# Performance work log

Measured on AMD Instinct MI355X. Metric: run time of the kernel, lower is better.

The kernel has to match this reference:

```python
import jax, jax.numpy as jnp
import numpy as np
from jax import lax

B, T, H, F, K, NB, MAXLEN = 32, 1024, 384, 384, 3, 256, 2048


def _ln(x, g, b, eps=1e-5):
    m = jnp.mean(x, axis=-1, keepdims=True)
    v = jnp.var(x, axis=-1, keepdims=True)
    return (x - m) * lax.rsqrt(v + eps) * g + b


def _conv(x, w, b):
    # x: (B, T, Cin), w: (K, Cin, Cout); SAME padding == torch padding=(K-1)//2 for K=3, stride 1
    y = lax.conv_general_dilated(x, w, (1,), 'SAME', dimension_numbers=('NWC', 'WIO', 'NWC'))
    return y + b


def _predictor(x, mask, w1, b1, g1, be1, w2, b2, g2, be2, wo, bo):
    h = _ln(jax.nn.relu(_conv(x, w1, b1)), g1, be1)
    h = _ln(jax.nn.relu(_conv(h, w2, b2)), g2, be2)
    out = jnp.einsum('btf,f->bt', h, wo) + bo  # Linear(F -> 1).squeeze(-1)
    return jnp.where(mask, 0.0, out)


def _length_regulate(x, dur, max_len):
    # vectorized equivalent of torch per-sample expand+cat+pad
    csum = jnp.cumsum(dur, axis=1)                      # (B, T)
    total = csum[:, -1]                                 # (B,) = mel_len
    frames = jnp.arange(max_len)                        # (M,)
    # frame f belongs to phoneme i with csum[i-1] <= f < csum[i]
    idx = jax.vmap(lambda c: jnp.searchsorted(c, frames, side='right'))(csum)  # (B, M)
    idx = jnp.clip(idx, 0, x.shape[1] - 1)
    out = jnp.take_along_axis(x, idx[:, :, None], axis=1)                      # (B, M, H)
    valid = (frames[None, :] < total[:, None]).astype(x.dtype)                 # zero-pad tail
    return out * valid[:, :, None], total


def setup_inputs() -> dict:
    key = jax.random.key(0)
    ks = iter(jax.random.split(key, 64))
    nk = lambda: next(ks)
    d = {}
    d['x'] = jax.random.normal(nk(), (B, T, H), jnp.float32)
    d['src_mask'] = jnp.zeros((B, T), jnp.bool_)
    d['duration'] = jax.random.randint(nk(), (B, T), 0, 4)
    d['max_len'] = MAXLEN
    for p in ('dp', 'pp', 'ep'):
        d[p + '_w1'] = jax.random.normal(nk(), (K, H, F), jnp.float32) * 0.02
        d[p + '_b1'] = jnp.zeros((F,), jnp.float32)
        d[p + '_g1'] = jnp.ones((F,), jnp.float32)
        d[p + '_be1'] = jnp.zeros((F,), jnp.float32)
        d[p + '_w2'] = jax.random.normal(nk(), (K, F, F), jnp.float32) * 0.02
        d[p + '_b2'] = jnp.zeros((F,), jnp.float32)
        d[p + '_g2'] = jnp.ones((F,), jnp.float32)
        d[p + '_be2'] = jnp.zeros((F,), jnp.float32)
        d[p + '_wo'] = jax.random.normal(nk(), (F,), jnp.float32) * 0.02
        d[p + '_bo'] = jnp.zeros((1,), jnp.float32)
    d['pitch_bins'] = jnp.linspace(0.0, 1.0, NB - 1, dtype=jnp.float32)
    d['energy_bins'] = jnp.linspace(0.0, 1.0, NB - 1, dtype=jnp.float32)
    d['pitch_emb'] = jax.random.normal(nk(), (NB, H), jnp.float32) * 0.02
    d['energy_emb'] = jax.random.normal(nk(), (NB, H), jnp.float32) * 0.02
    d['pitch_target'] = jax.random.uniform(nk(), (B, T), jnp.float32)
    d['energy_target'] = jax.random.uniform(nk(), (B, T), jnp.float32)
    return d


def reference(x, src_mask, duration, max_len,
              dp_w1, dp_b1, dp_g1, dp_be1, dp_w2, dp_b2, dp_g2, dp_be2, dp_wo, dp_bo,
              pp_w1, pp_b1, pp_g1, pp_be1, pp_w2, pp_b2, pp_g2, pp_be2, pp_wo, pp_bo,
              ep_w1, ep_b1, ep_g1, ep_be1, ep_w2, ep_b2, ep_g2, ep_be2, ep_wo, ep_bo,
              pitch_bins, energy_bins, pitch_emb, energy_emb, pitch_target, energy_target):
    log_dur = _predictor(x, src_mask, dp_w1, dp_b1, dp_g1, dp_be1, dp_w2, dp_b2, dp_g2, dp_be2, dp_wo, dp_bo)
    # phoneme-level pitch (target path: bucketize target, torch.bucketize right=False == searchsorted left)
    pitch_pred = _predictor(x, src_mask, pp_w1, pp_b1, pp_g1, pp_be1, pp_w2, pp_b2, pp_g2, pp_be2, pp_wo, pp_bo)
    x = x + pitch_emb[jnp.searchsorted(pitch_bins, pitch_target, side='left')]
    # phoneme-level energy (predictor sees x AFTER pitch embedding add, as in torch)
    energy_pred = _predictor(x, src_mask, ep_w1, ep_b1, ep_g1, ep_be1, ep_w2, ep_b2, ep_g2, ep_be2, ep_wo, ep_bo)
    x = x + energy_emb[jnp.searchsorted(energy_bins, energy_target, side='left')]
    x_out, mel_len = _length_regulate(x, duration, max_len)
    return (x_out, pitch_pred, energy_pred, log_dur, mel_len)
```

## Files before the change

kernel.cpp:

```cpp
#include <hip/hip_runtime.h>

#define B_ 32
#define T_ 1024
#define C_ 384
#define MAXLEN_ 2048
#define NBINS_ 255
#define WPK1 442368
#define BTC  (32 * 1024 * 384)
#define ARS 392

typedef __attribute__((ext_vector_type(8))) short short8v;
typedef __attribute__((ext_vector_type(4))) float floatx4;

__device__ __forceinline__ unsigned short f2bf(float f) {
    unsigned u = __float_as_uint(f);
    u += 0x7fffu + ((u >> 16) & 1u);
    return (unsigned short)(u >> 16);
}

struct CvP {
    const float* xf;
    const unsigned short* xb;
    const unsigned short* wpk;
    const float* bias[3];
    const float* gamma[3];
    const float* beta[3];
    const float* wo[3];
    const float* bo[3];
    unsigned short* hout;
    float* pred[3];
    const float* pbins;
    const float* pemb;
    const float* ptgt;
    int final_flag;
};

__global__ __launch_bounds__(512, 3) void conv_mfma3(CvP P)
{
    __shared__ unsigned short As[66 * ARS];
    __shared__ int embi[66];
    float* rsum = (float*)As;
    float* rsq  = rsum + 512;
    float* prbuf = rsum + 1024;

    const int tid  = threadIdx.x;
    const int wave = tid >> 6;
    const int lane = tid & 63;
    const int lq   = lane >> 4;
    const int ln   = lane & 15;
    const int p    = blockIdx.x >> 9;
    const int bi   = blockIdx.x & 511;
    const int b    = bi >> 4;
    const int t0   = (bi & 15) << 6;
    const int nb   = wave * 48;

    const unsigned short* bbase =
        P.wpk + (size_t)p * WPK1 + (size_t)(wave * 1536) + (size_t)lane * 8;
    short8v bA[3], bB[3];
#pragma unroll
    for (int nt = 0; nt < 3; ++nt) {
        bA[nt] = *(const short8v*)(bbase + (nt << 9));
        bB[nt] = *(const short8v*)(bbase + 12288 + (nt << 9));
    }

    if (!P.final_flag) {
        const bool fuse_emb = (p == 2);
        if (fuse_emb) {
            if (tid < 66) {
                const int t = t0 - 1 + tid;
                int lo = 0;
                if ((unsigned)t < (unsigned)T_) {
                    const float tg = P.ptgt[(b << 10) + t];
                    int hi = NBINS_;
                    while (lo < hi) {
                        const int mid = (lo + hi) >> 1;
                        if (P.pbins[mid] < tg) lo = mid + 1; else hi = mid;
                    }
                }
                embi[tid] = lo;
            }
            __syncthreads();
        }
        for (int i = tid; i < 66 * 96; i += 512) {
            const int row = i / 96;
            const int c4  = i - row * 96;
            const int t   = t0 - 1 + row;
            uint2 pv = make_uint2(0u, 0u);
            if ((unsigned)t < (unsigned)T_) {
                float4 f = *(const float4*)(P.xf + ((size_t)(b << 10) + t) * C_ + c4 * 4);
                if (fuse_emb) {
                    const float* er = P.pemb + (size_t)embi[row] * C_ + c4 * 4;
                    f.x += er[0]; f.y += er[1]; f.z += er[2]; f.w += er[3];
                }
                asm("v_cvt_pk_bf16_f32 %0, %1, %2" : "=v"(pv.x) : "v"(f.x), "v"(f.y));
                asm("v_cvt_pk_bf16_f32 %0, %1, %2" : "=v"(pv.y) : "v"(f.z), "v"(f.w));
            }
            *(uint2*)&As[row * ARS + c4 * 4] = pv;
        }
    } else {
        const unsigned short* xb = P.xb + (size_t)p * BTC;
        for (int i = tid; i < 66 * 48; i += 512) {
            const int row = i / 48;
            const int c   = i - row * 48;
            const int t   = t0 - 1 + row;
            short8v v = (short8v){0,0,0,0,0,0,0,0};
            if ((unsigned)t < (unsigned)T_)
                v = *(const short8v*)(xb + ((size_t)(b << 10) + t) * C_ + c * 8);
            *(short8v*)&As[row * ARS + c * 8] = v;
        }
    }
    __syncthreads();

    floatx4 acc[12];
#pragma unroll
    for (int i = 0; i < 12; ++i) acc[i] = (floatx4){0.f, 0.f, 0.f, 0.f};

    const unsigned short* abase = &As[ln * ARS + lq * 8];
    const unsigned short* bpA = bbase + 2 * 12288;
    const unsigned short* bpB = bbase + 3 * 12288;

#pragma unroll
    for (int kc = 0; kc < 3; ++kc) {
#pragma unroll
        for (int h2 = 0; h2 < 6; ++h2) {
            const int hb = h2 * 64;
            const int r  = kc * 12 + h2 * 2;
            {
                short8v afrag[4];
#pragma unroll
                for (int mt = 0; mt < 4; ++mt)
                    afrag[mt] = *(const short8v*)(abase + (mt * 16 + kc) * ARS + hb);
#pragma unroll
                for (int mt = 0; mt < 4; ++mt)
#pragma unroll
                    for (int nt = 0; nt < 3; ++nt)
                        acc[mt * 3 + nt] = __builtin_amdgcn_mfma_f32_16x16x32_bf16(
                            afrag[mt], bA[nt], acc[mt * 3 + nt], 0, 0, 0);
                if (r + 2 < 36) {
#pragma unroll
                    for (int nt = 0; nt < 3; ++nt)
                        bA[nt] = *(const short8v*)(bpA + (nt << 9));
                    bpA += 24576;
                }
            }
            {
                short8v afrag[4];
#pragma unroll
                for (int mt = 0; mt < 4; ++mt)
                    afrag[mt] = *(const short8v*)(abase + (mt * 16 + kc) * ARS + hb + 32);
#pragma unroll
                for (int mt = 0; mt < 4; ++mt)
#pragma unroll
                    for (int nt = 0; nt < 3; ++nt)
                        acc[mt * 3 + nt] = __builtin_amdgcn_mfma_f32_16x16x32_bf16(
                            afrag[mt], bB[nt], acc[mt * 3 + nt], 0, 0, 0);
                if (r + 3 < 36) {
#pragma unroll
                    for (int nt = 0; nt < 3; ++nt)
                        bB[nt] = *(const short8v*)(bpB + (nt << 9));
                    bpB += 24576;
                }
            }
        }
    }
    __syncthreads();

    float bcol[3], gcol[3], becol[3], wcol[3];
#pragma unroll
    for (int nt = 0; nt < 3; ++nt) {
        const int col = nb + nt * 16 + ln;
        bcol[nt]  = P.bias[p][col];
        gcol[nt]  = P.gamma[p][col];
        becol[nt] = P.beta[p][col];
        wcol[nt]  = P.final_flag ? P.wo[p][col] : 0.f;
    }

#pragma unroll
    for (int mt = 0; mt < 4; ++mt) {
#pragma unroll
        for (int rg = 0; rg < 4; ++rg) {
            float s = 0.f, q = 0.f;
#pragma unroll
            for (int nt = 0; nt < 3; ++nt) {
                float v = acc[mt * 3 + nt][rg] + bcol[nt];
                v = v > 0.f ? v : 0.f;
                acc[mt * 3 + nt][rg] = v;
                s += v; q += v * v;
            }
#pragma unroll
            for (int off = 1; off < 16; off <<= 1) {
                s += __shfl_xor(s, off, 64);
                q += __shfl_xor(q, off, 64);
            }
            if (ln == mt * 4 + rg) {
                rsum[wave * 64 + mt * 16 + lq * 4 + rg] = s;
                rsq [wave * 64 + mt * 16 + lq * 4 + rg] = q;
            }
        }
    }
    __syncthreads();

    if (!P.final_flag) {
        unsigned short* hout = P.hout + (size_t)p * BTC;
#pragma unroll
        for (int mt = 0; mt < 4; ++mt)
#pragma unroll
            for (int rg = 0; rg < 4; ++rg) {
                const int row = mt * 16 + lq * 4 + rg;
                float s = 0.f, q = 0.f;
#pragma unroll
                for (int w = 0; w < 8; ++w) {
                    s += rsum[w * 64 + row];
                    q += rsq [w * 64 + row];
                }
                const float m  = s * (1.f / 384.f);
                const float rs = rsqrtf(q * (1.f / 384.f) - m * m + 1e-5f);
                const int grow = (bi << 6) + row;
                unsigned short* hb_ = hout + (size_t)grow * C_ + nb + ln;
                const float v0 = (acc[mt * 3 + 0][rg] - m) * rs * gcol[0] + becol[0];
                const float v1 = (acc[mt * 3 + 1][rg] - m) * rs * gcol[1] + becol[1];
                const float v2 = (acc[mt * 3 + 2][rg] - m) * rs * gcol[2] + becol[2];
                unsigned u;
                asm("v_cvt_pk_bf16_f32 %0, %1, %2" : "=v"(u) : "v"(v0), "v"(v1));
                hb_[0]  = (unsigned short)(u & 0xffffu);
                hb_[16] = (unsigned short)(u >> 16);
                hb_[32] = f2bf(v2);
            }
    } else {
#pragma unroll
        for (int mt = 0; mt < 4; ++mt) {
#pragma unroll
            for (int rg = 0; rg < 4; ++rg) {
                const int row = mt * 16 + lq * 4 + rg;
                float s = 0.f, q = 0.f;
#pragma unroll
                for (int w = 0; w < 8; ++w) {
                    s += rsum[w * 64 + row];
                    q += rsq [w * 64 + row];
                }
                const float m  = s * (1.f / 384.f);
                const float rs = rsqrtf(q * (1.f / 384.f) - m * m + 1e-5f);
                float pr = 0.f;
#pragma unroll
                for (int nt = 0; nt < 3; ++nt)
                    pr += ((acc[mt * 3 + nt][rg] - m) * rs * gcol[nt] + becol[nt]) * wcol[nt];
#pragma unroll
                for (int off = 1; off < 16; off <<= 1)
                    pr += __shfl_xor(pr, off, 64);
                if (ln == mt * 4 + rg)
                    prbuf[wave * 64 + row] = pr;
            }
        }
        __syncthreads();
        if (tid < 64) {
            float s = P.bo[p][0];
#pragma unroll
            for (int w = 0; w < 8; ++w) s += prbuf[w * 64 + tid];
            P.pred[p][(bi << 6) + tid] = s;
        }
    }
}

#define WSS 388
__global__ __launch_bounds__(256) void pack_w_kernel(
    const float* __restrict__ s0, const float* __restrict__ s1,
    const float* __restrict__ s2, const float* __restrict__ s3,
    const float* __restrict__ s4, const float* __restrict__ s5,
    unsigned short* __restrict__ dst)
{
    __shared__ float ws[32 * WSS];
    const int blk  = blockIdx.x;
    const int wsel = blk / 36;
    const int r    = blk - wsel * 36;
    const float* src = wsel == 0 ? s0 : wsel == 1 ? s1 : wsel == 2 ? s2
                     : wsel == 3 ? s3 : wsel == 4 ? s4 : s5;
    const int tid = threadIdx.x;

    const float* sb = src + (size_t)r * 32 * C_;
    for (int i4 = tid; i4 < 3072; i4 += 256) {
        const int k  = i4 / 96;
        const int n4 = i4 - k * 96;
        *(float4*)&ws[k * WSS + n4 * 4] = *(const float4*)(sb + (size_t)k * C_ + n4 * 4);
    }
    __syncthreads();

    unsigned short* db = dst + (size_t)wsel * WPK1 + (size_t)r * 12288;
    for (int c = tid; c < 1536; c += 256) {
        const int lane = c & 63;
        const int wnt  = c >> 6;
        const int ln   = lane & 15;
        const int lq   = lane >> 4;
        const int n    = wnt * 16 + ln;
        ushort4 o0, o1;
        unsigned short e[8];
#pragma unroll
        for (int j = 0; j < 8; ++j)
            e[j] = f2bf(ws[(lq * 8 + j) * WSS + n]);
        o0 = make_ushort4(e[0], e[1], e[2], e[3]);
        o1 = make_ushort4(e[4], e[5], e[6], e[7]);
        *(ushort4*)(db + wnt * 512 + lane * 8)     = o0;
        *(ushort4*)(db + wnt * 512 + lane * 8 + 4) = o1;
    }
}

__global__ __launch_bounds__(256) void cumsum_idx_kernel(
    const int* __restrict__ dur,
    const float* __restrict__ pbins, const float* __restrict__ ptgt,
    const float* __restrict__ ebins, const float* __restrict__ etgt,
    int* __restrict__ xidx, float* __restrict__ mel_len)
{
    __shared__ int cs[T_];
    __shared__ int part[256];
    __shared__ float pb[NBINS_], eb[NBINS_];
    const int b = blockIdx.x;
    const int tid = threadIdx.x;
    if (tid < NBINS_) { pb[tid] = pbins[tid]; eb[tid] = ebins[tid]; }
    int l[4];
    int s = 0;
#pragma unroll
    for (int i = 0; i < 4; ++i) { l[i] = dur[(b << 10) + tid * 4 + i]; s += l[i]; }
    part[tid] = s;
    __syncthreads();
    for (int off = 1; off < 256; off <<= 1) {
        int u = 0;
        if (tid >= off) u = part[tid - off];
        __syncthreads();
        part[tid] += u;
        __syncthreads();
    }
    const int incl = part[tid];
    int run = incl - s;
#pragma unroll
    for (int i = 0; i < 4; ++i) {
        run += l[i];
        cs[tid * 4 + i] = run;
    }
    if (tid == 255) mel_len[b] = (float)incl;
    __syncthreads();
    const int total = cs[T_ - 1];
    for (int f = tid; f < MAXLEN_; f += 256) {
        int pk = -1;
        if (f < total) {
            int lo = 0, hi = T_;
            while (lo < hi) {
                const int mid = (lo + hi) >> 1;
                if (cs[mid] <= f) lo = mid + 1; else hi = mid;
            }
            const int t = lo > T_ - 1 ? T_ - 1 : lo;
            const int row = (b << 10) + t;
            const float ptg = ptgt[row];
            int plo = 0, phi = NBINS_;
            while (plo < phi) {
                const int mid = (plo + phi) >> 1;
                if (pb[mid] < ptg) plo = mid + 1; else phi = mid;
            }
            const float etg = etgt[row];
            int elo = 0, ehi = NBINS_;
            while (elo < ehi) {
                const int mid = (elo + ehi) >> 1;
                if (eb[mid] < etg) elo = mid + 1; else ehi = mid;
            }
            pk = t | (plo << 10) | (elo << 19);
        }
        xidx[(b << 11) + f] = pk;
    }
}

__global__ __launch_bounds__(256) void length_reg_kernel(
    const float* __restrict__ x, const int* __restrict__ xidx,
    const float* __restrict__ pemb, const float* __restrict__ eemb,
    float* __restrict__ out)
{
    const int g    = blockIdx.x * 256 + threadIdx.x;
    const int c4   = g % 96;
    const int rest = g / 96;
    const int frame = rest & (MAXLEN_ - 1);
    const int b     = rest >> 11;
    const int pk = xidx[(b << 11) + frame];
    float4 v = make_float4(0.f, 0.f, 0.f, 0.f);
    if (pk >= 0) {
        const int t   = pk & 1023;
        const int plo = (pk >> 10) & 511;
        const int elo = (pk >> 19) & 511;
        v = *(const float4*)(x + ((size_t)(b << 10) + t) * C_ + c4 * 4);
        const float4 pe = *(const float4*)(pemb + (size_t)plo * C_ + c4 * 4);
        const float4 ee = *(const float4*)(eemb + (size_t)elo * C_ + c4 * 4);
        v.x += pe.x + ee.x; v.y += pe.y + ee.y;
        v.z += pe.z + ee.z; v.w += pe.w + ee.w;
    }
    *(float4*)(out + (size_t)g * 4) = v;
}

extern "C" void kernel_launch(void* const* d_in, const int* in_sizes, int n_in,
                              void* d_out, int out_size, void* d_ws, size_t ws_size,
                              hipStream_t stream)
{
    const float* x        = (const float*)d_in[0];
    const int*   duration = (const int*)d_in[2];
    const float* P[3][10];
    for (int p = 0; p < 3; ++p)
        for (int q = 0; q < 10; ++q)
            P[p][q] = (const float*)d_in[4 + p * 10 + q];
    const float* pitch_bins    = (const float*)d_in[34];
    const float* energy_bins   = (const float*)d_in[35];
    const float* pitch_emb     = (const float*)d_in[36];
    const float* energy_emb    = (const float*)d_in[37];
    const float* pitch_target  = (const float*)d_in[38];
    const float* energy_target = (const float*)d_in[39];

    float* out_x      = (float*)d_out;
    float* out_pitch  = out_x + (size_t)B_ * MAXLEN_ * C_;
    float* out_energy = out_pitch + B_ * T_;
    float* out_logdur = out_energy + B_ * T_;
    float* out_mellen = out_logdur + B_ * T_;

    unsigned short* h1b = (unsigned short*)out_x;

    unsigned short* wpk = (unsigned short*)d_ws;
    int* xidx = (int*)(wpk + (size_t)6 * WPK1);

    const dim3 blk(256);
    const dim3 cblk(512);

    pack_w_kernel<<<216, blk, 0, stream>>>(
        P[0][0], P[0][4], P[1][0], P[1][4], P[2][0], P[2][4], wpk);

    CvP P1;
    P1.xf = x; P1.xb = nullptr; P1.wpk = wpk;
    for (int p = 0; p < 3; ++p) {
        P1.bias[p]  = P[p][1];
        P1.gamma[p] = P[p][2];
        P1.beta[p]  = P[p][3];
        P1.wo[p]    = nullptr;
        P1.bo[p]    = nullptr;
        P1.pred[p]  = nullptr;
    }
    P1.hout = h1b;
    P1.pbins = pitch_bins; P1.pemb = pitch_emb; P1.ptgt = pitch_target;
    P1.final_flag = 0;

    CvP P2;
    P2.xf = nullptr; P2.xb = h1b; P2.wpk = wpk + (size_t)3 * WPK1;
    for (int p = 0; p < 3; ++p) {
        P2.bias[p]  = P[p][5];
        P2.gamma[p] = P[p][6];
        P2.beta[p]  = P[p][7];
        P2.wo[p]    = P[p][8];
        P2.bo[p]    = P[p][9];
    }
    P2.pred[0] = out_logdur; P2.pred[1] = out_pitch; P2.pred[2] = out_energy;
    P2.hout = nullptr;
    P2.pbins = nullptr; P2.pemb = nullptr; P2.ptgt = nullptr;
    P2.final_flag = 1;

    conv_mfma3<<<1536, cblk, 0, stream>>>(P1);
    conv_mfma3<<<1536, cblk, 0, stream>>>(P2);

    cumsum_idx_kernel<<<B_, blk, 0, stream>>>(
        duration, pitch_bins, pitch_target, energy_bins, energy_target,
        xidx, out_mellen);
    length_reg_kernel<<<24576, blk, 0, stream>>>(
        x, xidx, pitch_emb, energy_emb, out_x);
}
```

Baseline: 472.3 us.

## Fuse both predictor conv layers into one kernel with halo recomputation

Merges the two conv+ReLU+LayerNorm stages into one kernel. The first conv is computed over 66 rows, two extra halo rows beyond the 64-row tile, and the normalized bf16 result is kept in shared memory as the second conv's input. This removes the global write and reload of the intermediate activations and one kernel launch. In exchange it does about 25% more first-layer MMA work and adds register pressure from the larger accumulator array.

```diff
diff --git a/kernel.cpp b/kernel.cpp
--- a/kernel.cpp
+++ b/kernel.cpp
@@ -6,8 +6,8 @@
 #define MAXLEN_ 2048
 #define NBINS_ 255
 #define WPK1 442368
-#define BTC  (32 * 1024 * 384)
 #define ARS 392
+#define AROWS 82
 
 typedef __attribute__((ext_vector_type(8))) short short8v;
 typedef __attribute__((ext_vector_type(4))) float floatx4;
@@ -20,28 +20,21 @@
 
 struct CvP {
     const float* xf;
-    const unsigned short* xb;
     const unsigned short* wpk;
-    const float* bias[3];
-    const float* gamma[3];
-    const float* beta[3];
-    const float* wo[3];
-    const float* bo[3];
-    unsigned short* hout;
+    const float* b1[3];  const float* g1[3];  const float* be1[3];
+    const float* b2[3];  const float* g2[3];  const float* be2[3];
+    const float* wo[3];  const float* bo[3];
     float* pred[3];
-    const float* pbins;
-    const float* pemb;
-    const float* ptgt;
-    int final_flag;
+    const float* pbins; const float* pemb; const float* ptgt;
 };
 
-__global__ __launch_bounds__(512, 3) void conv_mfma3(CvP P)
+__global__ __launch_bounds__(512, 3) void conv_fused3(CvP P)
 {
-    __shared__ unsigned short As[66 * ARS];
-    __shared__ int embi[66];
-    float* rsum = (float*)As;
-    float* rsq  = rsum + 512;
-    float* prbuf = rsum + 1024;
+    __shared__ unsigned short As[AROWS * ARS];
+    float* redS  = (float*)&As[68 * ARS];
+    float* redQ  = redS + 640;
+    float* prbuf = redQ + 640;
+    int*   embi  = (int*)(prbuf + 512);
 
     const int tid  = threadIdx.x;
     const int wave = tid >> 6;
@@ -54,137 +47,123 @@
     const int t0   = (bi & 15) << 6;
     const int nb   = wave * 48;
 
-    const unsigned short* bbase =
+    const unsigned short* b1base =
         P.wpk + (size_t)p * WPK1 + (size_t)(wave * 1536) + (size_t)lane * 8;
     short8v bA[3], bB[3];
 #pragma unroll
     for (int nt = 0; nt < 3; ++nt) {
-        bA[nt] = *(const short8v*)(bbase + (nt << 9));
-        bB[nt] = *(const short8v*)(bbase + 12288 + (nt << 9));
-    }
-
-    if (!P.final_flag) {
-        const bool fuse_emb = (p == 2);
-        if (fuse_emb) {
-            if (tid < 66) {
-                const int t = t0 - 1 + tid;
-                int lo = 0;
-                if ((unsigned)t < (unsigned)T_) {
-                    const float tg = P.ptgt[(b << 10) + t];
-                    int hi = NBINS_;
-                    while (lo < hi) {
-                        const int mid = (lo + hi) >> 1;
-                        if (P.pbins[mid] < tg) lo = mid + 1; else hi = mid;
+        bA[nt] = *(const short8v*)(b1base + (nt << 9));
+        bB[nt] = *(const short8v*)(b1base + 12288 + (nt << 9));
+    }
+
+    const bool fuse_emb = (p == 2);
+    if (fuse_emb) {
+        if (tid < 68) {
+            const int t = t0 - 2 + tid;
+            int lo = 0;
+            if ((unsigned)t < (unsigned)T_) {
+                const float tg = P.ptgt[(b << 10) + t];
+                int hi = NBINS_;
+                while (lo < hi) {
+                    const int mid = (lo + hi) >> 1;
+                    if (P.pbins[mid] < tg) lo = mid + 1; else hi = mid;
+                }
+            }
+            embi[tid] = lo;
+        }
+        __syncthreads();
+    }
+    for (int i = tid; i < 68 * 96; i += 512) {
+        const int row = i / 96;
+        const int c4  = i - row * 96;
+        const int t   = t0 - 2 + row;
+        uint2 pv = make_uint2(0u, 0u);
+        if ((unsigned)t < (unsigned)T_) {
+            float4 f = *(const float4*)(P.xf + ((size_t)(b << 10) + t) * C_ + c4 * 4);
+            if (fuse_emb) {
+                const float* er = P.pemb + (size_t)embi[row] * C_ + c4 * 4;
+                f.x += er[0]; f.y += er[1]; f.z += er[2]; f.w += er[3];
+            }
+            asm("v_cvt_pk_bf16_f32 %0, %1, %2" : "=v"(pv.x) : "v"(f.x), "v"(f.y));
+            asm("v_cvt_pk_bf16_f32 %0, %1, %2" : "=v"(pv.y) : "v"(f.z), "v"(f.w));
+        }
+        *(uint2*)&As[row * ARS + c4 * 4] = pv;
+    }
+    __syncthreads();
+
+    floatx4 acc1[15];
+#pragma unroll
+    for (int i = 0; i < 15; ++i) acc1[i] = (floatx4){0.f, 0.f, 0.f, 0.f};
+
+    const unsigned short* abase = &As[ln * ARS + lq * 8];
+    {
+        const unsigned short* bpA = b1base + 2 * 12288;
+        const unsigned short* bpB = b1base + 3 * 12288;
+#pragma unroll
+        for (int kc = 0; kc < 3; ++kc) {
+#pragma unroll
+            for (int h2 = 0; h2 < 6; ++h2) {
+                const int hb = h2 * 64;
+                const int r  = kc * 12 + h2 * 2;
+                {
+                    short8v afrag[5];
+#pragma unroll
+                    for (int mt = 0; mt < 5; ++mt)
+                        afrag[mt] = *(const short8v*)(abase + (mt * 16 + kc) * ARS + hb);
+#pragma unroll
+                    for (int mt = 0; mt < 5; ++mt)
+#pragma unroll
+                        for (int nt = 0; nt < 3; ++nt)
+                            acc1[mt * 3 + nt] = __builtin_amdgcn_mfma_f32_16x16x32_bf16(
+                                afrag[mt], bA[nt], acc1[mt * 3 + nt], 0, 0, 0);
+                    if (r + 2 < 36) {
+#pragma unroll
+                        for (int nt = 0; nt < 3; ++nt)
+                            bA[nt] = *(const short8v*)(bpA + (nt << 9));
+                        bpA += 24576;
                     }
                 }
-                embi[tid] = lo;
-            }
-            __syncthreads();
-        }
-        for (int i = tid; i < 66 * 96; i += 512) {
-            const int row = i / 96;
-            const int c4  = i - row * 96;
-            const int t   = t0 - 1 + row;
-            uint2 pv = make_uint2(0u, 0u);
-            if ((unsigned)t < (unsigned)T_) {
-                float4 f = *(const float4*)(P.xf + ((size_t)(b << 10) + t) * C_ + c4 * 4);
-                if (fuse_emb) {
-                    const float* er = P.pemb + (size_t)embi[row] * C_ + c4 * 4;
-                    f.x += er[0]; f.y += er[1]; f.z += er[2]; f.w += er[3];
-                }
-                asm("v_cvt_pk_bf16_f32 %0, %1, %2" : "=v"(pv.x) : "v"(f.x), "v"(f.y));
-                asm("v_cvt_pk_bf16_f32 %0, %1, %2" : "=v"(pv.y) : "v"(f.z), "v"(f.w));
-            }
-            *(uint2*)&As[row * ARS + c4 * 4] = pv;
-        }
-    } else {
-        const unsigned short* xb = P.xb + (size_t)p * BTC;
-        for (int i = tid; i < 66 * 48; i += 512) {
-            const int row = i / 48;
-            const int c   = i - row * 48;
-            const int t   = t0 - 1 + row;
-            short8v v = (short8v){0,0,0,0,0,0,0,0};
-            if ((unsigned)t < (unsigned)T_)
-                v = *(const short8v*)(xb + ((size_t)(b << 10) + t) * C_ + c * 8);
-            *(short8v*)&As[row * ARS + c * 8] = v;
-        }
-    }
-    __syncthreads();
-
-    floatx4 acc[12];
-#pragma unroll
-    for (int i = 0; i < 12; ++i) acc[i] = (floatx4){0.f, 0.f, 0.f, 0.f};
-
-    const unsigned short* abase = &As[ln * ARS + lq * 8];
-    const unsigned short* bpA = bbase + 2 * 12288;
-    const unsigned short* bpB = bbase + 3 * 12288;
-
-#pragma unroll
-    for (int kc = 0; kc < 3; ++kc) {
-#pragma unroll
-        for (int h2 = 0; h2 < 6; ++h2) {
-            const int hb = h2 * 64;
-            const int r  = kc * 12 + h2 * 2;
-            {
-                short8v afrag[4];
-#pragma unroll
-                for (int mt = 0; mt < 4; ++mt)
-                    afrag[mt] = *(const short8v*)(abase + (mt * 16 + kc) * ARS + hb);
-#pragma unroll
-                for (int mt = 0; mt < 4; ++mt)
-#pragma unroll
-                    for (int nt = 0; nt < 3; ++nt)
-                        acc[mt * 3 + nt] = __builtin_amdgcn_mfma_f32_16x16x32_bf16(
-                            afrag[mt], bA[nt], acc[mt * 3 + nt], 0, 0, 0);
-                if (r + 2 < 36) {
-#pragma unroll
-                    for (int nt = 0; nt < 3; ++nt)
-                        bA[nt] = *(const short8v*)(bpA + (nt << 9));
-                    bpA += 24576;
-                }
-            }
-            {
-                short8v afrag[4];
-#pragma unroll
-                for (int mt = 0; mt < 4; ++mt)
-                    afrag[mt] = *(const short8v*)(abase + (mt * 16 + kc) * ARS + hb + 32);
-#pragma unroll
-                for (int mt = 0; mt < 4; ++mt)
-#pragma unroll
-                    for (int nt = 0; nt < 3; ++nt)
-                        acc[mt * 3 + nt] = __builtin_amdgcn_mfma_f32_16x16x32_bf16(
-                            afrag[mt], bB[nt], acc[mt * 3 + nt], 0, 0, 0);
-                if (r + 3 < 36) {
-#pragma unroll
-                    for (int nt = 0; nt < 3; ++nt)
-                        bB[nt] = *(const short8v*)(bpB + (nt << 9));
-                    bpB += 24576;
-                }
-            }
-        }
-    }
-    __syncthreads();
-
-    float bcol[3], gcol[3], becol[3], wcol[3];
+                {
+                    short8v afrag[5];
+#pragma unroll
+                    for (int mt = 0; mt < 5; ++mt)
+                        afrag[mt] = *(const short8v*)(abase + (mt * 16 + kc) * ARS + hb + 32);
+#pragma unroll
+                    for (int mt = 0; mt < 5; ++mt)
+#pragma unroll
+                        for (int nt = 0; nt < 3; ++nt)
+                            acc1[mt * 3 + nt] = __builtin_amdgcn_mfma_f32_16x16x32_bf16(
+                                afrag[mt], bB[nt], acc1[mt * 3 + nt], 0, 0, 0);
+                    if (r + 3 < 36) {
+#pragma unroll
+                        for (int nt = 0; nt < 3; ++nt)
+                            bB[nt] = *(const short8v*)(bpB + (nt << 9));
+                        bpB += 24576;
+                    }
+                }
+            }
+        }
+    }
+    __syncthreads();
+
+    float c1b[3], c1g[3], c1be[3];
 #pragma unroll
     for (int nt = 0; nt < 3; ++nt) {
         const int col = nb + nt * 16 + ln;
-        bcol[nt]  = P.bias[p][col];
-        gcol[nt]  = P.gamma[p][col];
-        becol[nt] = P.beta[p][col];
-        wcol[nt]  = P.final_flag ? P.wo[p][col] : 0.f;
-    }
-
-#pragma unroll
-    for (int mt = 0; mt < 4; ++mt) {
+        c1b[nt]  = P.b1[p][col];
+        c1g[nt]  = P.g1[p][col];
+        c1be[nt] = P.be1[p][col];
+    }
+#pragma unroll
+    for (int mt = 0; mt < 5; ++mt) {
 #pragma unroll
         for (int rg = 0; rg < 4; ++rg) {
             float s = 0.f, q = 0.f;
 #pragma unroll
             for (int nt = 0; nt < 3; ++nt) {
-                float v = acc[mt * 3 + nt][rg] + bcol[nt];
+                float v = acc1[mt * 3 + nt][rg] + c1b[nt];
                 v = v > 0.f ? v : 0.f;
-                acc[mt * 3 + nt][rg] = v;
+                acc1[mt * 3 + nt][rg] = v;
                 s += v; q += v * v;
             }
 #pragma unroll
@@ -192,72 +171,165 @@
                 s += __shfl_xor(s, off, 64);
                 q += __shfl_xor(q, off, 64);
             }
-            if (ln == mt * 4 + rg) {
-                rsum[wave * 64 + mt * 16 + lq * 4 + rg] = s;
-                rsq [wave * 64 + mt * 16 + lq * 4 + rg] = q;
-            }
-        }
-    }
-    __syncthreads();
-
-    if (!P.final_flag) {
-        unsigned short* hout = P.hout + (size_t)p * BTC;
-#pragma unroll
-        for (int mt = 0; mt < 4; ++mt)
-#pragma unroll
-            for (int rg = 0; rg < 4; ++rg) {
-                const int row = mt * 16 + lq * 4 + rg;
+            if (ln == ((mt * 4 + rg) & 15)) {
+                redS[wave * 80 + mt * 16 + lq * 4 + rg] = s;
+                redQ[wave * 80 + mt * 16 + lq * 4 + rg] = q;
+            }
+        }
+    }
+    __syncthreads();
+
+#pragma unroll
+    for (int mt = 0; mt < 5; ++mt) {
+#pragma unroll
+        for (int rg = 0; rg < 4; ++rg) {
+            const int j = mt * 16 + lq * 4 + rg;
+            if (j < 66) {
+                const int th = t0 - 1 + j;
                 float s = 0.f, q = 0.f;
 #pragma unroll
                 for (int w = 0; w < 8; ++w) {
-                    s += rsum[w * 64 + row];
-                    q += rsq [w * 64 + row];
+                    s += redS[w * 80 + j];
+                    q += redQ[w * 80 + j];
                 }
                 const float m  = s * (1.f / 384.f);
                 const float rs = rsqrtf(q * (1.f / 384.f) - m * m + 1e-5f);
-                const int grow = (bi << 6) + row;
-                unsigned short* hb_ = hout + (size_t)grow * C_ + nb + ln;
-                const float v0 = (acc[mt * 3 + 0][rg] - m) * rs * gcol[0] + becol[0];
-                const float v1 = (acc[mt * 3 + 1][rg] - m) * rs * gcol[1] + becol[1];
-                const float v2 = (acc[mt * 3 + 2][rg] - m) * rs * gcol[2] + becol[2];
-                unsigned u;
-                asm("v_cvt_pk_bf16_f32 %0, %1, %2" : "=v"(u) : "v"(v0), "v"(v1));
-                hb_[0]  = (unsigned short)(u & 0xffffu);
-                hb_[16] = (unsigned short)(u >> 16);
-                hb_[32] = f2bf(v2);
-            }
-    } else {
-#pragma unroll
-        for (int mt = 0; mt < 4; ++mt) {
-#pragma unroll
-            for (int rg = 0; rg < 4; ++rg) {
-                const int row = mt * 16 + lq * 4 + rg;
-                float s = 0.f, q = 0.f;
-#pragma unroll
-                for (int w = 0; w < 8; ++w) {
-                    s += rsum[w * 64 + row];
-                    q += rsq [w * 64 + row];
-                }
-                const float m  = s * (1.f / 384.f);
-                const float rs = rsqrtf(q * (1.f / 384.f) - m * m + 1e-5f);
-                float pr = 0.f;
-#pragma unroll
-                for (int nt = 0; nt < 3; ++nt)
-                    pr += ((acc[mt * 3 + nt][rg] - m) * rs * gcol[nt] + becol[nt]) * wcol[nt];
-#pragma unroll
-                for (int off = 1; off < 16; off <<= 1)
-                    pr += __shfl_xor(pr, off, 64);
-                if (ln == mt * 4 + rg)
-                    prbuf[wave * 64 + row] = pr;
-            }
-        }
-        __syncthreads();
-        if (tid < 64) {
-            float s = P.bo[p][0];
-#pragma unroll
-            for (int w = 0; w < 8; ++w) s += prbuf[w * 64 + tid];
-            P.pred[p][(bi << 6) + tid] = s;
-        }
+                const bool valid = (unsigned)th < (unsigned)T_;
+#pragma unroll
+                for (int nt = 0; nt < 3; ++nt) {
+                    float v = (acc1[mt * 3 + nt][rg] - m) * rs * c1g[nt] + c1be[nt];
+                    if (!valid) v = 0.f;
+                    As[j * ARS + nb + nt * 16 + ln] = f2bf(v);
+                }
+            }
+        }
+    }
+
+    const unsigned short* b2base =
+        P.wpk + (size_t)(3 + p) * WPK1 + (size_t)(wave * 1536) + (size_t)lane * 8;
+#pragma unroll
+    for (int nt = 0; nt < 3; ++nt) {
+        bA[nt] = *(const short8v*)(b2base + (nt << 9));
+        bB[nt] = *(const short8v*)(b2base + 12288 + (nt << 9));
+    }
+    __syncthreads();
+
+    floatx4 acc2[12];
+#pragma unroll
+    for (int i = 0; i < 12; ++i) acc2[i] = (floatx4){0.f, 0.f, 0.f, 0.f};
+    {
+        const unsigned short* bpA = b2base + 2 * 12288;
+        const unsigned short* bpB = b2base + 3 * 12288;
+#pragma unroll
+        for (int kc = 0; kc < 3; ++kc) {
+#pragma unroll
+            for (int h2 = 0; h2 < 6; ++h2) {
+                const int hb = h2 * 64;
+                const int r  = kc * 12 + h2 * 2;
+                {
+                    short8v afrag[4];
+#pragma unroll
+                    for (int mt = 0; mt < 4; ++mt)
+                        afrag[mt] = *(const short8v*)(abase + (mt * 16 + kc) * ARS + hb);
+#pragma unroll
+                    for (int mt = 0; mt < 4; ++mt)
+#pragma unroll
+                        for (int nt = 0; nt < 3; ++nt)
+                            acc2[mt * 3 + nt] = __builtin_amdgcn_mfma_f32_16x16x32_bf16(
+                                afrag[mt], bA[nt], acc2[mt * 3 + nt], 0, 0, 0);
+                    if (r + 2 < 36) {
+#pragma unroll
+                        for (int nt = 0; nt < 3; ++nt)
+                            bA[nt] = *(const short8v*)(bpA + (nt << 9));
+                        bpA += 24576;
+                    }
+                }
+                {
+                    short8v afrag[4];
+#pragma unroll
+                    for (int mt = 0; mt < 4; ++mt)
+                        afrag[mt] = *(const short8v*)(abase + (mt * 16 + kc) * ARS + hb + 32);
+#pragma unroll
+                    for (int mt = 0; mt < 4; ++mt)
+#pragma unroll
+                        for (int nt = 0; nt < 3; ++nt)
+                            acc2[mt * 3 + nt] = __builtin_amdgcn_mfma_f32_16x16x32_bf16(
+                                afrag[mt], bB[nt], acc2[mt * 3 + nt], 0, 0, 0);
+                    if (r + 3 < 36) {
+#pragma unroll
+                        for (int nt = 0; nt < 3; ++nt)
+                            bB[nt] = *(const short8v*)(bpB + (nt << 9));
+                        bpB += 24576;
+                    }
+                }
+            }
+        }
+    }
+
+    float c2b[3], c2g[3], c2be[3], cwo[3];
+#pragma unroll
+    for (int nt = 0; nt < 3; ++nt) {
+        const int col = nb + nt * 16 + ln;
+        c2b[nt]  = P.b2[p][col];
+        c2g[nt]  = P.g2[p][col];
+        c2be[nt] = P.be2[p][col];
+        cwo[nt]  = P.wo[p][col];
+    }
+#pragma unroll
+    for (int mt = 0; mt < 4; ++mt) {
+#pragma unroll
+        for (int rg = 0; rg < 4; ++rg) {
+            float s = 0.f, q = 0.f;
+#pragma unroll
+            for (int nt = 0; nt < 3; ++nt) {
+                float v = acc2[mt * 3 + nt][rg] + c2b[nt];
+                v = v > 0.f ? v : 0.f;
+                acc2[mt * 3 + nt][rg] = v;
+                s += v; q += v * v;
+            }
+#pragma unroll
+            for (int off = 1; off < 16; off <<= 1) {
+                s += __shfl_xor(s, off, 64);
+                q += __shfl_xor(q, off, 64);
+            }
+            if (ln == ((mt * 4 + rg) & 15)) {
+                redS[wave * 80 + mt * 16 + lq * 4 + rg] = s;
+                redQ[wave * 80 + mt * 16 + lq * 4 + rg] = q;
+            }
+        }
+    }
+    __syncthreads();
+
+#pragma unroll
+    for (int mt = 0; mt < 4; ++mt) {
+#pragma unroll
+        for (int rg = 0; rg < 4; ++rg) {
+            const int row = mt * 16 + lq * 4 + rg;
+            float s = 0.f, q = 0.f;
+#pragma unroll
+            for (int w = 0; w < 8; ++w) {
+                s += redS[w * 80 + row];
+                q += redQ[w * 80 + row];
+            }
+            const float m  = s * (1.f / 384.f);
+            const float rs = rsqrtf(q * (1.f / 384.f) - m * m + 1e-5f);
+            float pr = 0.f;
+#pragma unroll
+            for (int nt = 0; nt < 3; ++nt)
+                pr += ((acc2[mt * 3 + nt][rg] - m) * rs * c2g[nt] + c2be[nt]) * cwo[nt];
+#pragma unroll
+            for (int off = 1; off < 16; off <<= 1)
+                pr += __shfl_xor(pr, off, 64);
+            if (ln == ((mt * 4 + rg) & 15))
+                prbuf[wave * 64 + row] = pr;
+        }
+    }
+    __syncthreads();
+    if (tid < 64) {
+        float s = P.bo[p][0];
+#pragma unroll
+        for (int w = 0; w < 8; ++w) s += prbuf[w * 64 + tid];
+        P.pred[p][(bi << 6) + tid] = s;
     }
 }
 
@@ -414,8 +486,6 @@
     float* out_logdur = out_energy + B_ * T_;
     float* out_mellen = out_logdur + B_ * T_;
 
-    unsigned short* h1b = (unsigned short*)out_x;
-
     unsigned short* wpk = (unsigned short*)d_ws;
     int* xidx = (int*)(wpk + (size_t)6 * WPK1);
 
@@ -425,36 +495,22 @@
     pack_w_kernel<<<216, blk, 0, stream>>>(
         P[0][0], P[0][4], P[1][0], P[1][4], P[2][0], P[2][4], wpk);
 
-    CvP P1;
-    P1.xf = x; P1.xb = nullptr; P1.wpk = wpk;
+    CvP Pa;
+    Pa.xf = x; Pa.wpk = wpk;
     for (int p = 0; p < 3; ++p) {
-        P1.bias[p]  = P[p][1];
-        P1.gamma[p] = P[p][2];
-        P1.beta[p]  = P[p][3];
-        P1.wo[p]    = nullptr;
-        P1.bo[p]    = nullptr;
-        P1.pred[p]  = nullptr;
-    }
-    P1.hout = h1b;
-    P1.pbins = pitch_bins; P1.pemb = pitch_emb; P1.ptgt = pitch_target;
-    P1.final_flag = 0;
-
-    CvP P2;
-    P2.xf = nullptr; P2.xb = h1b; P2.wpk = wpk + (size_t)3 * WPK1;
-    for (int p = 0; p < 3; ++p) {
-        P2.bias[p]  = P[p][5];
-        P2.gamma[p] = P[p][6];
-        P2.beta[p]  = P[p][7];
-        P2.wo[p]    = P[p][8];
-        P2.bo[p]    = P[p][9];
-    }
-    P2.pred[0] = out_logdur; P2.pred[1] = out_pitch; P2.pred[2] = out_energy;
-    P2.hout = nullptr;
-    P2.pbins = nullptr; P2.pemb = nullptr; P2.ptgt = nullptr;
-    P2.final_flag = 1;
-
-    conv_mfma3<<<1536, cblk, 0, stream>>>(P1);
-    conv_mfma3<<<1536, cblk, 0, stream>>>(P2);
+        Pa.b1[p]  = P[p][1];
+        Pa.g1[p]  = P[p][2];
+        Pa.be1[p] = P[p][3];
+        Pa.b2[p]  = P[p][5];
+        Pa.g2[p]  = P[p][6];
+        Pa.be2[p] = P[p][7];
+        Pa.wo[p]  = P[p][8];
+        Pa.bo[p]  = P[p][9];
+    }
+    Pa.pred[0] = out_logdur; Pa.pred[1] = out_pitch; Pa.pred[2] = out_energy;
+    Pa.pbins = pitch_bins; Pa.pemb = pitch_emb; Pa.ptgt = pitch_target;
+
+    conv_fused3<<<1536, cblk, 0, stream>>>(Pa);
 
     cumsum_idx_kernel<<<B_, blk, 0, stream>>>(
         duration, pitch_bins, pitch_target, energy_bins, energy_target,
```

After: 522.4 us. 10.6% more time.
